# Optimization experiments

Hardware: AMD Instinct MI355X
Metric: run time of the kernel (lower is better)

Reference implementation:

```python
import jax, jax.numpy as jnp
import numpy as np

N = 20000
E = 320000
F_IN = 256
HID = 32
HEADS = 8
EDGE_DIM = HID // 4  # 8
NEG_SLOPE = 0.2


def _gat_conv(x, src, dst, e_emb, W, att_s, att_d, W_e, att_e, bias, H, C):
    """PyG-style GATConv with edge_dim, add_self_loops=True (fill_value='mean'), concat heads."""
    n = x.shape[0]
    loop = jnp.arange(n, dtype=src.dtype)
    # self-loop edge_attr = scatter-mean of edge_attr by dst (0 for isolated nodes)
    deg = jax.ops.segment_sum(jnp.ones_like(dst, dtype=x.dtype), dst, num_segments=n)
    e_mean = jax.ops.segment_sum(e_emb, dst, num_segments=n) / jnp.maximum(deg, 1.0)[:, None]
    src_a = jnp.concatenate([src, loop])
    dst_a = jnp.concatenate([dst, loop])
    e_all = jnp.concatenate([e_emb, e_mean], axis=0)  # [E+N, edge_dim]

    h = (x @ W).reshape(n, H, C)                      # [N,H,C]
    a_src = jnp.einsum('nhc,hc->nh', h, att_s)        # [N,H]
    a_dst = jnp.einsum('nhc,hc->nh', h, att_d)
    he = (e_all @ W_e).reshape(-1, H, C)              # [E+N,H,C]
    a_edge = jnp.einsum('ehc,hc->eh', he, att_e)      # [E+N,H]

    alpha = jax.nn.leaky_relu(a_src[src_a] + a_dst[dst_a] + a_edge, NEG_SLOPE)
    # segment softmax over destination nodes
    amax = jax.ops.segment_max(alpha, dst_a, num_segments=n)
    alpha = jnp.exp(alpha - amax[dst_a])
    denom = jax.ops.segment_sum(alpha, dst_a, num_segments=n)
    alpha = alpha / (denom[dst_a] + 1e-16)

    msg = h[src_a] * alpha[:, :, None]                # [E+N,H,C]
    out = jax.ops.segment_sum(msg, dst_a, num_segments=n)  # [N,H,C]
    return out.reshape(n, H * C) + bias


def setup_inputs() -> dict:
    key = jax.random.key(0)
    ks = jax.random.split(key, 16)

    def glorot(k, shape):
        fan_in, fan_out = shape[0], shape[-1]
        s = np.sqrt(6.0 / (fan_in + fan_out))
        return jax.random.uniform(k, shape, jnp.float32, -s, s)

    x = jax.random.normal(ks[0], (N, F_IN), jnp.float32)
    edge_index = jax.random.randint(ks[1], (2, E), 0, N, jnp.int32)
    edge_attr = jax.random.uniform(ks[2], (E, 2), jnp.float32)

    # spatial_embed: Linear(2 -> EDGE_DIM)
    Wse = glorot(ks[3], (2, EDGE_DIM))
    bse = jnp.zeros((EDGE_DIM,), jnp.float32)
    # conv1: in=F_IN, heads=HEADS, out=HID, edge_dim=EDGE_DIM
    W1 = glorot(ks[4], (F_IN, HEADS * HID))
    as1 = glorot(ks[5], (HEADS, HID))
    ad1 = glorot(ks[6], (HEADS, HID))
    We1 = glorot(ks[7], (EDGE_DIM, HEADS * HID))
    ae1 = glorot(ks[8], (HEADS, HID))
    b1 = jnp.zeros((HEADS * HID,), jnp.float32)
    # conv2: in=HEADS*HID, heads=1, out=HID
    W2 = glorot(ks[9], (HEADS * HID, HID))
    as2 = glorot(ks[10], (1, HID))
    ad2 = glorot(ks[11], (1, HID))
    We2 = glorot(ks[12], (EDGE_DIM, HID))
    ae2 = glorot(ks[13], (1, HID))
    b2 = jnp.zeros((HID,), jnp.float32)

    return {"x": x, "edge_index": edge_index, "edge_attr": edge_attr,
            "Wse": Wse, "bse": bse,
            "W1": W1, "as1": as1, "ad1": ad1, "We1": We1, "ae1": ae1, "b1": b1,
            "W2": W2, "as2": as2, "ad2": ad2, "We2": We2, "ae2": ae2, "b2": b2}


def reference(x, edge_index, edge_attr, Wse, bse,
              W1, as1, ad1, We1, ae1, b1,
              W2, as2, ad2, We2, ae2, b2):
    src, dst = edge_index[0], edge_index[1]
    e = jax.nn.relu(edge_attr @ Wse + bse)            # [E, EDGE_DIM]
    h = _gat_conv(x, src, dst, e, W1, as1, ad1, We1, ae1, b1, HEADS, HID)
    h = jax.nn.relu(h)                                # dropout inactive (eval)
    out = _gat_conv(h, src, dst, e, W2, as2, ad2, We2, ae2, b2, 1, HID)
    return out
```

## Files before the change

kernel.cpp:

```cpp
#include <hip/hip_runtime.h>
#include <float.h>


typedef short v8s __attribute__((ext_vector_type(8)));
typedef float v4f __attribute__((ext_vector_type(4)));

__device__ __forceinline__ ushort f2bf(float f) {
  unsigned u = __float_as_uint(f);
  u = (u + 0x7FFF + ((u >> 16) & 1)) >> 16;
  return (ushort)u;
}
__device__ __forceinline__ float bf2f(ushort h) {
  return __uint_as_float(((unsigned)h) << 16);
}

__global__ __launch_bounds__(1024) void k_scan(const int* __restrict__ deg,
                                               int* __restrict__ row_ptr, int N) {
  __shared__ int part[1024];
  int tid = threadIdx.x;
  int chunk = (N + 1023) / 1024;
  int lo = tid * chunk;
  if (lo > N) lo = N;
  int hi = lo + chunk;
  if (hi > N) hi = N;
  int s = 0;
  for (int i = lo; i < hi; i++) s += deg[i] + 1;
  part[tid] = s;
  __syncthreads();
  for (int off = 1; off < 1024; off <<= 1) {
    int v = 0;
    if (tid >= off) v = part[tid - off];
    __syncthreads();
    part[tid] += v;
    __syncthreads();
  }
  int base = part[tid] - s;
  for (int i = lo; i < hi; i++) { row_ptr[i] = base; base += deg[i] + 1; }
  if (tid == 1023) row_ptr[N] = part[1023];
}

__global__ void k_scatter(const int* __restrict__ src, const int* __restrict__ dst,
                          const int* __restrict__ row_ptr, int* __restrict__ cursor,
                          const float* __restrict__ aed1_lin, const float* __restrict__ aed2_lin,
                          int* __restrict__ csr_src, float* __restrict__ csr_aed1,
                          float* __restrict__ csr_aed2, int* __restrict__ selfpos,
                          int E, int N) {
  int i = blockIdx.x * blockDim.x + threadIdx.x;
  if (i >= E + N) return;
  if (i < E) {
    int d = dst[i];
    int pos = row_ptr[d] + atomicAdd(&cursor[d], 1);
    csr_src[pos] = src[i];
    const float4* a4 = (const float4*)(aed1_lin + (size_t)i * 8);
    *(float4*)(csr_aed1 + (size_t)pos * 8)     = a4[0];
    *(float4*)(csr_aed1 + (size_t)pos * 8 + 4) = a4[1];
    csr_aed2[pos] = aed2_lin[i];
  } else {
    int n = i - E;
    int pos = row_ptr[n] + atomicAdd(&cursor[n], 1);
    csr_src[pos] = n;
    selfpos[n] = pos;
  }
}

__global__ __launch_bounds__(256) void k_prep_trans(const float* __restrict__ W1,
                                                    const float* __restrict__ We1,
                                                    const float* __restrict__ ae1,
                                                    const float* __restrict__ We2,
                                                    const float* __restrict__ ae2,
                                                    ushort* __restrict__ Bt,
                                                    float* __restrict__ M1,
                                                    float* __restrict__ m2) {
  if (blockIdx.x == 64) {
    int t = threadIdx.x;
    if (t < 64) {
      int k = t >> 3, h = t & 7;
      float s = 0.f;
      for (int c = 0; c < 32; c++) s += We1[k * 256 + h * 32 + c] * ae1[h * 32 + c];
      M1[k * 8 + h] = s;
    } else if (t < 72) {
      int k = t - 64;
      float s = 0.f;
      for (int c = 0; c < 32; c++) s += We2[k * 32 + c] * ae2[c];
      m2[k] = s;
    }
    return;
  }
  __shared__ float tile[32][33];
  int bx = blockIdx.x & 7, by = blockIdx.x >> 3;
  int tx = threadIdx.x & 31, ty = threadIdx.x >> 5;
  for (int r = ty; r < 32; r += 8)
    tile[r][tx] = W1[(size_t)(by * 32 + r) * 256 + bx * 32 + tx];
  __syncthreads();
  for (int r = ty; r < 32; r += 8)
    Bt[(size_t)(bx * 32 + r) * 256 + by * 32 + tx] = f2bf(tile[tx][r]);
}

__global__ void k_edge_fused(const float* __restrict__ ea, const int* __restrict__ dst,
                             const float* __restrict__ Wse, const float* __restrict__ bse,
                             const float* __restrict__ M1, const float* __restrict__ m2,
                             float* __restrict__ aed1, float* __restrict__ aed2,
                             int* __restrict__ deg, int E) {
  __shared__ float sW[16], sb[8], sM[64], sm2[8];
  int t = threadIdx.x;
  if (t < 16) sW[t] = Wse[t];
  if (t < 8) sb[t] = bse[t];
  if (t < 64) sM[t] = M1[t];
  if (t >= 64 && t < 72) sm2[t - 64] = m2[t - 64];
  __syncthreads();
  int e = blockIdx.x * blockDim.x + t;
  if (e >= E) return;
  atomicAdd(&deg[dst[e]], 1);
  float2 av = ((const float2*)ea)[e];
  float e8[8];
#pragma unroll
  for (int k = 0; k < 8; k++)
    e8[k] = fmaxf(av.x * sW[k] + av.y * sW[8 + k] + sb[k], 0.f);
  float o[8];
#pragma unroll
  for (int h = 0; h < 8; h++) {
    float s = 0.f;
#pragma unroll
    for (int k = 0; k < 8; k++) s += e8[k] * sM[k * 8 + h];
    o[h] = s;
  }
  *(float4*)(aed1 + (size_t)e * 8)     = make_float4(o[0], o[1], o[2], o[3]);
  *(float4*)(aed1 + (size_t)e * 8 + 4) = make_float4(o[4], o[5], o[6], o[7]);
  float s2 = 0.f;
#pragma unroll
  for (int k = 0; k < 8; k++) s2 += e8[k] * sm2[k];
  aed2[e] = s2;
}

__global__ void k_selfmean(const int* __restrict__ row_ptr, const int* __restrict__ selfpos,
                           float* __restrict__ csr_aed1, float* __restrict__ csr_aed2,
                           int N) {
  int i = blockIdx.x * blockDim.x + threadIdx.x;
  if (i >= N * 8) return;
  int n = i >> 3, h = i & 7;
  int begin = row_ptr[n], end = row_ptr[n + 1];
  int sp = selfpos[n];
  int deg = end - begin - 1;
  float inv = 1.f / (float)(deg > 1 ? deg : 1);
  float s = 0.f, s2 = 0.f;
  for (int p = begin; p < end; p++) {
    if (p == sp) continue;
    s += csr_aed1[(size_t)p * 8 + h];
    if (h == 0) s2 += csr_aed2[p];
  }
  csr_aed1[(size_t)sp * 8 + h] = s * inv;
  if (h == 0) csr_aed2[sp] = s2 * inv;
}

__global__ __launch_bounds__(256) void k_gemm1_mfma(const float* __restrict__ A,
                                                    const ushort* __restrict__ Bt,
                                                    const float* __restrict__ as1,
                                                    const float* __restrict__ ad1,
                                                    ushort* __restrict__ h1b,
                                                    float* __restrict__ asv,
                                                    float* __restrict__ adv, int M) {
  __shared__ ushort sA[64 * 40];
  __shared__ ushort sB[256 * 40];
  __shared__ float sas[256], sad[256];
  int t = threadIdx.x;
  int wave = t >> 6, lane = t & 63;
  int m0 = blockIdx.x * 64;
  int c = lane & 15, kg = lane >> 4;
  sas[t] = as1[t];
  sad[t] = ad1[t];
  v4f acc[4][4];
#pragma unroll
  for (int a = 0; a < 4; a++)
#pragma unroll
    for (int b = 0; b < 4; b++) acc[a][b] = (v4f)(0.f);
  int arow = t >> 2;
  int akoff = (t & 3) * 8;
  bool aval = (m0 + arow) < M;
  const float* aptr = A + (size_t)(m0 + arow) * 256 + akoff;
  const ushort* bptr = Bt + (size_t)t * 256;
  for (int k0 = 0; k0 < 256; k0 += 32) {
    float4 v0 = make_float4(0.f, 0.f, 0.f, 0.f), v1 = v0;
    if (aval) { v0 = *(const float4*)(aptr + k0); v1 = *(const float4*)(aptr + k0 + 4); }
    ushort* dst = &sA[arow * 40 + akoff];
    dst[0] = f2bf(v0.x); dst[1] = f2bf(v0.y); dst[2] = f2bf(v0.z); dst[3] = f2bf(v0.w);
    dst[4] = f2bf(v1.x); dst[5] = f2bf(v1.y); dst[6] = f2bf(v1.z); dst[7] = f2bf(v1.w);
    *(v8s*)&sB[t * 40 + 0]  = *(const v8s*)(bptr + k0 + 0);
    *(v8s*)&sB[t * 40 + 8]  = *(const v8s*)(bptr + k0 + 8);
    *(v8s*)&sB[t * 40 + 16] = *(const v8s*)(bptr + k0 + 16);
    *(v8s*)&sB[t * 40 + 24] = *(const v8s*)(bptr + k0 + 24);
    __syncthreads();
    v8s af[4], bfr[4];
#pragma unroll
    for (int mt = 0; mt < 4; mt++) af[mt] = *(v8s*)&sA[(mt * 16 + c) * 40 + kg * 8];
#pragma unroll
    for (int nt = 0; nt < 4; nt++) bfr[nt] = *(v8s*)&sB[(wave * 64 + nt * 16 + c) * 40 + kg * 8];
#pragma unroll
    for (int mt = 0; mt < 4; mt++)
#pragma unroll
      for (int nt = 0; nt < 4; nt++)
        acc[mt][nt] = __builtin_amdgcn_mfma_f32_16x16x32_bf16(af[mt], bfr[nt], acc[mt][nt], 0, 0, 0);
    __syncthreads();
  }
  int colbase = wave * 64;
#pragma unroll
  for (int mt = 0; mt < 4; mt++) {
#pragma unroll
    for (int i = 0; i < 4; i++) {
      int m = m0 + mt * 16 + kg * 4 + i;
      if (m < M) {
#pragma unroll
        for (int nt = 0; nt < 4; nt++)
          h1b[(size_t)m * 256 + colbase + nt * 16 + c] = f2bf(acc[mt][nt][i]);
      }
      float s1a = acc[mt][0][i] * sas[colbase + c]      + acc[mt][1][i] * sas[colbase + 16 + c];
      float s2a = acc[mt][0][i] * sad[colbase + c]      + acc[mt][1][i] * sad[colbase + 16 + c];
      float s1b = acc[mt][2][i] * sas[colbase + 32 + c] + acc[mt][3][i] * sas[colbase + 48 + c];
      float s2b = acc[mt][2][i] * sad[colbase + 32 + c] + acc[mt][3][i] * sad[colbase + 48 + c];
#pragma unroll
      for (int o = 1; o < 16; o <<= 1) {
        s1a += __shfl_xor(s1a, o);
        s2a += __shfl_xor(s2a, o);
        s1b += __shfl_xor(s1b, o);
        s2b += __shfl_xor(s2b, o);
      }
      if (c == 0 && m < M) {
        asv[(size_t)m * 8 + 2 * wave]     = s1a;
        adv[(size_t)m * 8 + 2 * wave]     = s2a;
        asv[(size_t)m * 8 + 2 * wave + 1] = s1b;
        adv[(size_t)m * 8 + 2 * wave + 1] = s2b;
      }
    }
  }
}

__global__ __launch_bounds__(64) void k_conv1(
    const int* __restrict__ row_ptr, const int* __restrict__ csr_src,
    const float* __restrict__ csr_aed1, const float* __restrict__ asv,
    const float* __restrict__ adv, const ushort* __restrict__ h1b,
    const float* __restrict__ b1, ushort* __restrict__ h2b, int N) {
  int n = blockIdx.x;
  int lane = threadIdx.x;
  int h = lane >> 3;
  int sub = lane & 7;
  __shared__ float sw[64 * 8];
  __shared__ int ssrc[64];
  __shared__ float sm[8], sl[8], sadv[8];
  int begin = row_ptr[n], end = row_ptr[n + 1];
  if (lane < 8) { sm[lane] = -FLT_MAX; sl[lane] = 0.f; sadv[lane] = adv[(size_t)n * 8 + lane]; }
  float4 acc = make_float4(0.f, 0.f, 0.f, 0.f);
  for (int cs = begin; cs < end; cs += 64) {
    int c = min(64, end - cs);
    __syncthreads();
    if (lane < c) ssrc[lane] = csr_src[cs + lane];
    __syncthreads();
    for (int idx = lane; idx < c * 8; idx += 64) {
      int el = idx >> 3, hh = idx & 7;
      float a = asv[(size_t)ssrc[el] * 8 + hh] + sadv[hh] +
                csr_aed1[(size_t)(cs + el) * 8 + hh];
      a = a > 0.f ? a : 0.2f * a;
      sw[idx] = a;
    }
    __syncthreads();
    float mloc = -FLT_MAX;
    for (int el = sub; el < c; el += 8) mloc = fmaxf(mloc, sw[el * 8 + h]);
#pragma unroll
    for (int o = 1; o < 8; o <<= 1) mloc = fmaxf(mloc, __shfl_xor(mloc, o));
    float mold = sm[h];
    float mnew = fmaxf(mold, mloc);
    float scale = __expf(mold - mnew);
    float lloc = 0.f;
    for (int el = sub; el < c; el += 8) {
      float w = __expf(sw[el * 8 + h] - mnew);
      sw[el * 8 + h] = w;
      lloc += w;
    }
#pragma unroll
    for (int o = 1; o < 8; o <<= 1) lloc += __shfl_xor(lloc, o);
    __syncthreads();
    if (sub == 0) { sm[h] = mnew; sl[h] = sl[h] * scale + lloc; }
    acc.x *= scale; acc.y *= scale; acc.z *= scale; acc.w *= scale;
    for (int el = 0; el < c; el++) {
      float w = sw[el * 8 + h];
      ushort4 hv = *(const ushort4*)(h1b + (size_t)ssrc[el] * 256 + lane * 4);
      acc.x += w * bf2f(hv.x);
      acc.y += w * bf2f(hv.y);
      acc.z += w * bf2f(hv.z);
      acc.w += w * bf2f(hv.w);
    }
  }
  __syncthreads();
  float inv = 1.f / (sl[h] + 1e-16f);
  float4 bv = *(const float4*)(b1 + lane * 4);
  ushort4 o4;
  o4.x = f2bf(fmaxf(acc.x * inv + bv.x, 0.f));
  o4.y = f2bf(fmaxf(acc.y * inv + bv.y, 0.f));
  o4.z = f2bf(fmaxf(acc.z * inv + bv.z, 0.f));
  o4.w = f2bf(fmaxf(acc.w * inv + bv.w, 0.f));
  *(ushort4*)(h2b + (size_t)n * 256 + lane * 4) = o4;
}

__global__ __launch_bounds__(256) void k_gemm2(const ushort* __restrict__ h2b,
                                               const float* __restrict__ W2,
                                               const float* __restrict__ as2,
                                               const float* __restrict__ ad2,
                                               float* __restrict__ g2,
                                               float* __restrict__ asv2,
                                               float* __restrict__ adv2, int N) {
  __shared__ float xs[8 * 256];
  __shared__ float sas[32], sad[32];
  int t = threadIdx.x;
  if (t < 32) { sas[t] = as2[t]; sad[t] = ad2[t]; }
  int n0 = blockIdx.x * 8;
  for (int idx = t; idx < 8 * 256; idx += 256) {
    int node = n0 + (idx >> 8);
    xs[idx] = (node < N) ? bf2f(h2b[(size_t)node * 256 + (idx & 255)]) : 0.f;
  }
  __syncthreads();
  int j = t >> 5, cc = t & 31;
  int node = n0 + j;
  float acc = 0.f;
#pragma unroll 8
  for (int k = 0; k < 256; k++) acc += xs[j * 256 + k] * W2[k * 32 + cc];
  float s1 = acc * sas[cc], s2 = acc * sad[cc];
#pragma unroll
  for (int o = 1; o < 32; o <<= 1) {
    s1 += __shfl_xor(s1, o);
    s2 += __shfl_xor(s2, o);
  }
  if (node < N) {
    g2[(size_t)node * 32 + cc] = acc;
    if (cc == 0) { asv2[node] = s1; adv2[node] = s2; }
  }
}

__global__ __launch_bounds__(64) void k_conv2(
    const int* __restrict__ row_ptr, const int* __restrict__ csr_src,
    const float* __restrict__ csr_aed2, const float* __restrict__ asv2,
    const float* __restrict__ adv2, const float* __restrict__ g2,
    const float* __restrict__ b2, float* __restrict__ out, int N) {
  int n = blockIdx.x;
  int lane = threadIdx.x;
  int sub = lane >> 3, q = lane & 7;
  __shared__ float sw[64];
  __shared__ int ssrc[64];
  int begin = row_ptr[n], end = row_ptr[n + 1];
  float advn = adv2[n];
  float m = -FLT_MAX, l = 0.f;
  float4 acc = make_float4(0.f, 0.f, 0.f, 0.f);
  for (int cs = begin; cs < end; cs += 64) {
    int c = min(64, end - cs);
    __syncthreads();
    float a = -FLT_MAX;
    if (lane < c) {
      int s = csr_src[cs + lane];
      ssrc[lane] = s;
      a = asv2[s] + advn + csr_aed2[cs + lane];
      a = a > 0.f ? a : 0.2f * a;
    }
    float cm = a;
#pragma unroll
    for (int o = 1; o < 64; o <<= 1) cm = fmaxf(cm, __shfl_xor(cm, o));
    float nm = fmaxf(m, cm);
    float sc = __expf(m - nm);
    float w = (lane < c) ? __expf(a - nm) : 0.f;
    float cl = w;
#pragma unroll
    for (int o = 1; o < 64; o <<= 1) cl += __shfl_xor(cl, o);
    l = l * sc + cl;
    m = nm;
    sw[lane] = w;
    __syncthreads();
    acc.x *= sc; acc.y *= sc; acc.z *= sc; acc.w *= sc;
    for (int el = sub; el < c; el += 8) {
      float w2 = sw[el];
      const float4 gv = *(const float4*)(g2 + (size_t)ssrc[el] * 32 + q * 4);
      acc.x += w2 * gv.x; acc.y += w2 * gv.y; acc.z += w2 * gv.z; acc.w += w2 * gv.w;
    }
  }
#pragma unroll
  for (int o = 8; o < 64; o <<= 1) {
    acc.x += __shfl_xor(acc.x, o);
    acc.y += __shfl_xor(acc.y, o);
    acc.z += __shfl_xor(acc.z, o);
    acc.w += __shfl_xor(acc.w, o);
  }
  if (lane < 8) {
    float inv = 1.f / (l + 1e-16f);
    float4 bv = *(const float4*)(b2 + lane * 4);
    float4 o4;
    o4.x = acc.x * inv + bv.x;
    o4.y = acc.y * inv + bv.y;
    o4.z = acc.z * inv + bv.z;
    o4.w = acc.w * inv + bv.w;
    *(float4*)(out + (size_t)n * 32 + lane * 4) = o4;
  }
}

extern "C" void kernel_launch(void* const* d_in, const int* in_sizes, int n_in,
                              void* d_out, int out_size, void* d_ws, size_t ws_size,
                              hipStream_t stream) {
  (void)n_in; (void)out_size; (void)ws_size;
  const float* x   = (const float*)d_in[0];
  const int*   ei  = (const int*)d_in[1];
  const float* ea  = (const float*)d_in[2];
  const float* Wse = (const float*)d_in[3];
  const float* bse = (const float*)d_in[4];
  const float* W1  = (const float*)d_in[5];
  const float* as1 = (const float*)d_in[6];
  const float* ad1 = (const float*)d_in[7];
  const float* We1 = (const float*)d_in[8];
  const float* ae1 = (const float*)d_in[9];
  const float* b1  = (const float*)d_in[10];
  const float* W2  = (const float*)d_in[11];
  const float* as2 = (const float*)d_in[12];
  const float* ad2 = (const float*)d_in[13];
  const float* We2 = (const float*)d_in[14];
  const float* ae2 = (const float*)d_in[15];
  const float* b2  = (const float*)d_in[16];
  const int N = in_sizes[0] / 256;
  const int E = in_sizes[1] / 2;
  const int* src = ei;
  const int* dst = ei + E;

  char* base = (char*)d_ws;
  size_t off = 0;
  auto alloc = [&](size_t bytes) -> char* {
    off = (off + 255) & ~(size_t)255;
    char* p = base + off;
    off += bytes;
    return p;
  };
  int*   deg      = (int*)alloc((size_t)N * 4);
  int*   cursor   = (int*)alloc((size_t)N * 4);
  size_t zero_bytes = (size_t)((char*)(cursor + N) - (char*)deg);
  int* row_ptr    = (int*)alloc((size_t)(N + 1) * 4);
  int* selfpos    = (int*)alloc((size_t)N * 4);
  int* csr_src    = (int*)alloc((size_t)(E + N) * 4);
  float* aed1_lin = (float*)alloc((size_t)E * 8 * 4);
  float* aed2_lin = (float*)alloc((size_t)E * 4);
  float* csr_aed1 = (float*)alloc((size_t)(E + N) * 8 * 4);
  float* csr_aed2 = (float*)alloc((size_t)(E + N) * 4);
  ushort* W1T     = (ushort*)alloc((size_t)256 * 256 * 2);
  ushort* h1b     = (ushort*)alloc((size_t)N * 256 * 2);
  float* asv1     = (float*)alloc((size_t)N * 8 * 4);
  float* adv1     = (float*)alloc((size_t)N * 8 * 4);
  ushort* h2b     = (ushort*)alloc((size_t)N * 256 * 2);
  float* g2       = (float*)alloc((size_t)N * 32 * 4);
  float* asv2     = (float*)alloc((size_t)N * 4);
  float* adv2     = (float*)alloc((size_t)N * 4);
  float* M1       = (float*)alloc(64 * 4);
  float* m2       = (float*)alloc(8 * 4);

  hipMemsetAsync(deg, 0, zero_bytes, stream);
  k_prep_trans<<<65, 256, 0, stream>>>(W1, We1, ae1, We2, ae2, W1T, M1, m2);
  k_edge_fused<<<(E + 255) / 256, 256, 0, stream>>>(ea, dst, Wse, bse, M1, m2,
                                                    aed1_lin, aed2_lin, deg, E);
  k_scan<<<1, 1024, 0, stream>>>(deg, row_ptr, N);
  k_scatter<<<(E + N + 255) / 256, 256, 0, stream>>>(src, dst, row_ptr, cursor,
                                                     aed1_lin, aed2_lin,
                                                     csr_src, csr_aed1, csr_aed2, selfpos, E, N);
  k_selfmean<<<(N * 8 + 255) / 256, 256, 0, stream>>>(row_ptr, selfpos, csr_aed1, csr_aed2, N);
  k_gemm1_mfma<<<(N + 63) / 64, 256, 0, stream>>>(x, W1T, as1, ad1, h1b, asv1, adv1, N);
  k_conv1<<<N, 64, 0, stream>>>(row_ptr, csr_src, csr_aed1, asv1, adv1, h1b, b1, h2b, N);
  k_gemm2<<<(N + 7) / 8, 256, 0, stream>>>(h2b, W2, as2, ad2, g2, asv2, adv2, N);
  k_conv2<<<N, 64, 0, stream>>>(row_ptr, csr_src, csr_aed2, asv2, adv2, g2, b2, (float*)d_out, N);
}
```

Before: 266.9 us.

## Handle self-loops analytically inside conv kernels, drop selfmean kernel

Removes self-loop entries from the CSR and deletes the separate self-mean kernel. Each conv kernel now accumulates the sum of edge attention terms while it walks the neighbour list, forms the mean for the self-loop, and folds the self-loop term into the online softmax at the end. This eliminates one kernel launch, a serial per-node pass over the CSR, and the N extra scatter entries and atomics. The cost is some extra per-node work in the conv epilogue and a different floating-point summation order.

```diff
diff --git a/kernel.cpp b/kernel.cpp
--- a/kernel.cpp
+++ b/kernel.cpp
@@ -24,7 +24,7 @@
   int hi = lo + chunk;
   if (hi > N) hi = N;
   int s = 0;
-  for (int i = lo; i < hi; i++) s += deg[i] + 1;
+  for (int i = lo; i < hi; i++) s += deg[i];
   part[tid] = s;
   __syncthreads();
   for (int off = 1; off < 1024; off <<= 1) {
@@ -35,7 +35,7 @@
     __syncthreads();
   }
   int base = part[tid] - s;
-  for (int i = lo; i < hi; i++) { row_ptr[i] = base; base += deg[i] + 1; }
+  for (int i = lo; i < hi; i++) { row_ptr[i] = base; base += deg[i]; }
   if (tid == 1023) row_ptr[N] = part[1023];
 }
 
@@ -43,24 +43,16 @@
                           const int* __restrict__ row_ptr, int* __restrict__ cursor,
                           const float* __restrict__ aed1_lin, const float* __restrict__ aed2_lin,
                           int* __restrict__ csr_src, float* __restrict__ csr_aed1,
-                          float* __restrict__ csr_aed2, int* __restrict__ selfpos,
-                          int E, int N) {
+                          float* __restrict__ csr_aed2, int E) {
   int i = blockIdx.x * blockDim.x + threadIdx.x;
-  if (i >= E + N) return;
-  if (i < E) {
-    int d = dst[i];
-    int pos = row_ptr[d] + atomicAdd(&cursor[d], 1);
-    csr_src[pos] = src[i];
-    const float4* a4 = (const float4*)(aed1_lin + (size_t)i * 8);
-    *(float4*)(csr_aed1 + (size_t)pos * 8)     = a4[0];
-    *(float4*)(csr_aed1 + (size_t)pos * 8 + 4) = a4[1];
-    csr_aed2[pos] = aed2_lin[i];
-  } else {
-    int n = i - E;
-    int pos = row_ptr[n] + atomicAdd(&cursor[n], 1);
-    csr_src[pos] = n;
-    selfpos[n] = pos;
-  }
+  if (i >= E) return;
+  int d = dst[i];
+  int pos = row_ptr[d] + atomicAdd(&cursor[d], 1);
+  csr_src[pos] = src[i];
+  const float4* a4 = (const float4*)(aed1_lin + (size_t)i * 8);
+  *(float4*)(csr_aed1 + (size_t)pos * 8)     = a4[0];
+  *(float4*)(csr_aed1 + (size_t)pos * 8 + 4) = a4[1];
+  csr_aed2[pos] = aed2_lin[i];
 }
 
 __global__ __launch_bounds__(256) void k_prep_trans(const float* __restrict__ W1,
@@ -132,26 +124,6 @@
   aed2[e] = s2;
 }
 
-__global__ void k_selfmean(const int* __restrict__ row_ptr, const int* __restrict__ selfpos,
-                           float* __restrict__ csr_aed1, float* __restrict__ csr_aed2,
-                           int N) {
-  int i = blockIdx.x * blockDim.x + threadIdx.x;
-  if (i >= N * 8) return;
-  int n = i >> 3, h = i & 7;
-  int begin = row_ptr[n], end = row_ptr[n + 1];
-  int sp = selfpos[n];
-  int deg = end - begin - 1;
-  float inv = 1.f / (float)(deg > 1 ? deg : 1);
-  float s = 0.f, s2 = 0.f;
-  for (int p = begin; p < end; p++) {
-    if (p == sp) continue;
-    s += csr_aed1[(size_t)p * 8 + h];
-    if (h == 0) s2 += csr_aed2[p];
-  }
-  csr_aed1[(size_t)sp * 8 + h] = s * inv;
-  if (h == 0) csr_aed2[sp] = s2 * inv;
-}
-
 __global__ __launch_bounds__(256) void k_gemm1_mfma(const float* __restrict__ A,
                                                     const ushort* __restrict__ Bt,
                                                     const float* __restrict__ as1,
@@ -242,11 +214,14 @@
   int lane = threadIdx.x;
   int h = lane >> 3;
   int sub = lane & 7;
+  int hh = lane & 7;
   __shared__ float sw[64 * 8];
   __shared__ int ssrc[64];
-  __shared__ float sm[8], sl[8], sadv[8];
+  __shared__ float sm[8], sl[8], sadv[8], smean[8];
   int begin = row_ptr[n], end = row_ptr[n + 1];
+  int degr = end - begin;
   if (lane < 8) { sm[lane] = -FLT_MAX; sl[lane] = 0.f; sadv[lane] = adv[(size_t)n * 8 + lane]; }
+  float aedsum = 0.f;
   float4 acc = make_float4(0.f, 0.f, 0.f, 0.f);
   for (int cs = begin; cs < end; cs += 64) {
     int c = min(64, end - cs);
@@ -254,9 +229,10 @@
     if (lane < c) ssrc[lane] = csr_src[cs + lane];
     __syncthreads();
     for (int idx = lane; idx < c * 8; idx += 64) {
-      int el = idx >> 3, hh = idx & 7;
-      float a = asv[(size_t)ssrc[el] * 8 + hh] + sadv[hh] +
-                csr_aed1[(size_t)(cs + el) * 8 + hh];
+      int el = idx >> 3;
+      float ae = csr_aed1[(size_t)(cs + el) * 8 + hh];
+      aedsum += ae;
+      float a = asv[(size_t)ssrc[el] * 8 + hh] + sadv[hh] + ae;
       a = a > 0.f ? a : 0.2f * a;
       sw[idx] = a;
     }
@@ -288,8 +264,25 @@
       acc.w += w * bf2f(hv.w);
     }
   }
+  aedsum += __shfl_xor(aedsum, 8);
+  aedsum += __shfl_xor(aedsum, 16);
+  aedsum += __shfl_xor(aedsum, 32);
+  float invd = 1.f / (float)(degr > 1 ? degr : 1);
+  if (lane < 8) smean[lane] = aedsum * invd;
   __syncthreads();
-  float inv = 1.f / (sl[h] + 1e-16f);
+  float a_self = asv[(size_t)n * 8 + h] + sadv[h] + smean[h];
+  a_self = a_self > 0.f ? a_self : 0.2f * a_self;
+  float mold = sm[h];
+  float mnew = fmaxf(mold, a_self);
+  float scale = __expf(mold - mnew);
+  float w_self = __expf(a_self - mnew);
+  float l_fin = sl[h] * scale + w_self;
+  ushort4 hs = *(const ushort4*)(h1b + (size_t)n * 256 + lane * 4);
+  acc.x = acc.x * scale + w_self * bf2f(hs.x);
+  acc.y = acc.y * scale + w_self * bf2f(hs.y);
+  acc.z = acc.z * scale + w_self * bf2f(hs.z);
+  acc.w = acc.w * scale + w_self * bf2f(hs.w);
+  float inv = 1.f / (l_fin + 1e-16f);
   float4 bv = *(const float4*)(b1 + lane * 4);
   ushort4 o4;
   o4.x = f2bf(fmaxf(acc.x * inv + bv.x, 0.f));
@@ -344,8 +337,9 @@
   __shared__ float sw[64];
   __shared__ int ssrc[64];
   int begin = row_ptr[n], end = row_ptr[n + 1];
+  int degr = end - begin;
   float advn = adv2[n];
-  float m = -FLT_MAX, l = 0.f;
+  float m = -FLT_MAX, l = 0.f, aedsum = 0.f;
   float4 acc = make_float4(0.f, 0.f, 0.f, 0.f);
   for (int cs = begin; cs < end; cs += 64) {
     int c = min(64, end - cs);
@@ -354,7 +348,9 @@
     if (lane < c) {
       int s = csr_src[cs + lane];
       ssrc[lane] = s;
-      a = asv2[s] + advn + csr_aed2[cs + lane];
+      float ae = csr_aed2[cs + lane];
+      aedsum += ae;
+      a = asv2[s] + advn + ae;
       a = a > 0.f ? a : 0.2f * a;
     }
     float cm = a;
@@ -376,6 +372,21 @@
       const float4 gv = *(const float4*)(g2 + (size_t)ssrc[el] * 32 + q * 4);
       acc.x += w2 * gv.x; acc.y += w2 * gv.y; acc.z += w2 * gv.z; acc.w += w2 * gv.w;
     }
+  }
+#pragma unroll
+  for (int o = 1; o < 64; o <<= 1) aedsum += __shfl_xor(aedsum, o);
+  float invd = 1.f / (float)(degr > 1 ? degr : 1);
+  float a_self = asv2[n] + advn + aedsum * invd;
+  a_self = a_self > 0.f ? a_self : 0.2f * a_self;
+  float nm = fmaxf(m, a_self);
+  float sc = __expf(m - nm);
+  float w_self = __expf(a_self - nm);
+  l = l * sc + w_self;
+  acc.x *= sc; acc.y *= sc; acc.z *= sc; acc.w *= sc;
+  if (sub == 0) {
+    const float4 gv = *(const float4*)(g2 + (size_t)n * 32 + q * 4);
+    acc.x += w_self * gv.x; acc.y += w_self * gv.y;
+    acc.z += w_self * gv.z; acc.w += w_self * gv.w;
   }
 #pragma unroll
   for (int o = 8; o < 64; o <<= 1) {
@@ -434,12 +445,11 @@
   int*   cursor   = (int*)alloc((size_t)N * 4);
   size_t zero_bytes = (size_t)((char*)(cursor + N) - (char*)deg);
   int* row_ptr    = (int*)alloc((size_t)(N + 1) * 4);
-  int* selfpos    = (int*)alloc((size_t)N * 4);
-  int* csr_src    = (int*)alloc((size_t)(E + N) * 4);
+  int* csr_src    = (int*)alloc((size_t)E * 4);
   float* aed1_lin = (float*)alloc((size_t)E * 8 * 4);
   float* aed2_lin = (float*)alloc((size_t)E * 4);
-  float* csr_aed1 = (float*)alloc((size_t)(E + N) * 8 * 4);
-  float* csr_aed2 = (float*)alloc((size_t)(E + N) * 4);
+  float* csr_aed1 = (float*)alloc((size_t)E * 8 * 4);
+  float* csr_aed2 = (float*)alloc((size_t)E * 4);
   ushort* W1T     = (ushort*)alloc((size_t)256 * 256 * 2);
   ushort* h1b     = (ushort*)alloc((size_t)N * 256 * 2);
   float* asv1     = (float*)alloc((size_t)N * 8 * 4);
@@ -456,12 +466,12 @@
   k_edge_fused<<<(E + 255) / 256, 256, 0, stream>>>(ea, dst, Wse, bse, M1, m2,
                                                     aed1_lin, aed2_lin, deg, E);
   k_scan<<<1, 1024, 0, stream>>>(deg, row_ptr, N);
-  k_scatter<<<(E + N + 255) / 256, 256, 0, stream>>>(src, dst, row_ptr, cursor,
-                                                     aed1_lin, aed2_lin,
-                                                     csr_src, csr_aed1, csr_aed2, selfpos, E, N);
-  k_selfmean<<<(N * 8 + 255) / 256, 256, 0, stream>>>(row_ptr, selfpos, csr_aed1, csr_aed2, N);
+  k_scatter<<<(E + 255) / 256, 256, 0, stream>>>(src, dst, row_ptr, cursor,
+                                                 aed1_lin, aed2_lin,
+                                                 csr_src, csr_aed1, csr_aed2, E);
   k_gemm1_mfma<<<(N + 63) / 64, 256, 0, stream>>>(x, W1T, as1, ad1, h1b, asv1, adv1, N);
   k_conv1<<<N, 64, 0, stream>>>(row_ptr, csr_src, csr_aed1, asv1, adv1, h1b, b1, h2b, N);
   k_gemm2<<<(N + 7) / 8, 256, 0, stream>>>(h2b, W2, as2, ad2, g2, asv2, adv2, N);
-  k_conv2<<<N, 64, 0, stream>>>(row_ptr, csr_src, csr_aed2, asv2, adv2, g2, b2, (float*)d_out, N);
-}
+  k_conv2<<<N, 64, 0, stream>>>(row_ptr, csr_src, csr_aed2, asv2, adv2, g2, b2,
+                                (float*)d_out, N);
+}
```

Result: faster. 258.3 us (-3.2%).
